# Performance work log

Measured on AMD Instinct MI355X. Metric: run time of the kernel, lower is better.

Reference implementation:

```python
import jax, jax.numpy as jnp
import numpy as np
from jax import lax

V1 = 12001   # vocab_size + 1
E = 300      # input_encoding_size
R = 1024     # rnn_size
H = 512      # att_hid_size
F = 2048     # att_feat_size
B = 64
T = 20
L = 196      # number of attention regions (14x14)


def setup_inputs() -> dict:
    key = jax.random.key(0)
    ks = jax.random.split(key, 12)
    s = 0.02
    return {
        "seq": jax.random.randint(ks[0], (B, T), 0, V1),
        "att_feats": jax.random.normal(ks[1], (B, L, F), dtype=jnp.float32),
        "embed_w": jax.random.uniform(ks[2], (V1, E), minval=-0.1, maxval=0.1),
        "ctx2att_w": jax.random.normal(ks[3], (H, F)) * s,
        "ctx2att_b": jnp.zeros((H,)),
        "h2att_w": jax.random.normal(ks[4], (H, R)) * s,
        "h2att_b": jnp.zeros((H,)),
        "alpha_w": jax.random.normal(ks[5], (1, H)) * s,
        "alpha_b": jnp.zeros((1,)),
        "i2h_w": jax.random.normal(ks[6], (5 * R, E)) * s,
        "i2h_b": jnp.zeros((5 * R,)),
        "h2h_w": jax.random.normal(ks[7], (5 * R, R)) * s,
        "h2h_b": jnp.zeros((5 * R,)),
        "a2c_w": jax.random.normal(ks[8], (2 * R, F)) * s,
        "a2c_b": jnp.zeros((2 * R,)),
        "logit_w": jax.random.uniform(ks[9], (V1, R), minval=-0.1, maxval=0.1),
        "logit_b": jnp.zeros((V1,)),
    }


def reference(seq, att_feats, embed_w, ctx2att_w, ctx2att_b, h2att_w, h2att_b,
              alpha_w, alpha_b, i2h_w, i2h_b, h2h_w, h2h_b, a2c_w, a2c_b,
              logit_w, logit_b):
    # Eval-mode dropout (identity). Faithful to core()/lstm() math.
    Bq, Tq = seq.shape
    Rr = h2h_w.shape[1]
    # p_att_feats is recomputed identically per step in the original; hoist it.
    p_att = att_feats @ ctx2att_w.T + ctx2att_b            # [B, L, H]

    def step(carry, it):
        h, c = carry
        xt = embed_w[it]                                    # [B, E]
        # additive (Bahdanau) attention over L regions
        att_h = h @ h2att_w.T + h2att_b                     # [B, H]
        dot = jnp.tanh(p_att + att_h[:, None, :])           # [B, L, H]
        e = jnp.einsum('blh,h->bl', dot, alpha_w[0]) + alpha_b[0]
        w = jax.nn.softmax(e, axis=-1)                      # [B, L]
        att_res = jnp.einsum('bl,blf->bf', w, att_feats)    # [B, F]
        # LSTM cell with maxout in_transform and context gating via a2c
        sums = xt @ i2h_w.T + i2h_b + h @ h2h_w.T + h2h_b   # [B, 5R]
        sg = jax.nn.sigmoid(sums[:, :3 * Rr])
        in_g, fg, og = sg[:, :Rr], sg[:, Rr:2 * Rr], sg[:, 2 * Rr:3 * Rr]
        itr = sums[:, 3 * Rr:] + att_res @ a2c_w.T + a2c_b  # [B, 2R]
        g = jnp.maximum(itr[:, :Rr], itr[:, Rr:])
        nc = fg * c + in_g * g
        nh = og * jnp.tanh(nc)
        logp = jax.nn.log_softmax(nh @ logit_w.T + logit_b, axis=-1)
        return (nh, nc), logp

    h0 = jnp.zeros((Bq, Rr), dtype=att_feats.dtype)
    _, logps = lax.scan(step, (h0, h0), seq.T)              # [T, B, V+1]
    return jnp.transpose(logps, (1, 0, 2))                  # [B, T, V+1]
```

## Files before the change

kernel.cpp:

```cpp
#include <hip/hip_runtime.h>
#include <math.h>

namespace {
constexpr int kV = 12001;
constexpr int kE = 300;
constexpr int kEp = 320;
constexpr int kR = 1024;
constexpr int kH = 512;
constexpr int kF = 2048;
constexpr int kB = 64;
constexpr int kT = 20;
constexpr int kL = 196;
constexpr int kNcat = 5 * kR + kH;
constexpr int kKS = 4;
constexpr int kNc2 = kH + kF;
}

typedef __attribute__((ext_vector_type(8))) short short8;
typedef __attribute__((ext_vector_type(4))) float f32x4;

#define GLB_PTR(p) ((const __attribute__((address_space(1))) void*)(p))
#define LDS_PTR(p) ((__attribute__((address_space(3))) void*)(p))

__device__ __forceinline__ unsigned short f2bf(float f) {
    unsigned u = __builtin_bit_cast(unsigned, f);
    u = (u + 0x7fffu + ((u >> 16) & 1u)) >> 16;
    return (unsigned short)u;
}
__device__ __forceinline__ float bf2f(unsigned short h) {
    unsigned u = ((unsigned)h) << 16;
    return __builtin_bit_cast(float, u);
}
__device__ __forceinline__ float fast_tanh(float x) {
    x = fminf(15.f, fmaxf(-15.f, x));
    const float e = __expf(2.f * x);
    return (e - 1.f) / (e + 1.f);
}
__device__ __forceinline__ float fast_sig(float x) {
    return 1.f / (1.f + __expf(-x));
}

__device__ __forceinline__ int xcd_swizzle(int orig, int nwg) {
    const int q = nwg >> 3, r = nwg & 7;
    const int xcd = orig & 7, lo = orig >> 3;
    return (xcd < r ? xcd * (q + 1) : r * (q + 1) + (xcd - r) * q) + lo;
}

__global__ __launch_bounds__(256)
void conv_all_kernel(const float* __restrict__ af_in,  unsigned short* __restrict__ af_out,
                     const float* __restrict__ ctx_in,
                     const float* __restrict__ lg_in,  unsigned short* __restrict__ lg_out,
                     const float* __restrict__ h2h_in, unsigned short* __restrict__ h2h_out,
                     const float* __restrict__ h2a_in, unsigned short* __restrict__ h2a_out,
                     const float* __restrict__ a2c_in, unsigned short* __restrict__ wcomb_out,
                     const float* __restrict__ emb_in, unsigned short* __restrict__ emb_out,
                     const float* __restrict__ i2h_in, unsigned short* __restrict__ i2h_out,
                     unsigned short* __restrict__ hz_out, float* __restrict__ cb_out,
                     const float* __restrict__ ctxb_in, const float* __restrict__ a2cb_in,
                     float* __restrict__ biasc_out)
{
    constexpr int c0 = kB * kL * kF / 4;
    constexpr int c1 = c0 + kH * kF / 4;
    constexpr int c2 = c1 + kV * kR / 4;
    constexpr int c3 = c2 + 5 * kR * kR / 4;
    constexpr int c4 = c3 + kH * kR / 4;
    constexpr int c5 = c4 + 2 * kR * kF / 4;
    constexpr int c6 = c5 + kV * 80;
    constexpr int c7 = c6 + 5 * kR * 80;
    constexpr int c8 = c7 + kB * kR / 4;
    constexpr int c9 = c8 + kB * kR / 4;
    constexpr int c10 = c9 + kNc2 / 4;

    for (int i = blockIdx.x * 256 + threadIdx.x; i < c10; i += gridDim.x * 256) {
        if (i < c4) {
            const float* in; unsigned short* out; int l;
            if      (i < c0) { in = af_in;  out = af_out;    l = i; }
            else if (i < c1) { in = ctx_in; out = wcomb_out; l = i - c0; }
            else if (i < c2) { in = lg_in;  out = lg_out;    l = i - c1; }
            else if (i < c3) { in = h2h_in; out = h2h_out;   l = i - c2; }
            else             { in = h2a_in; out = h2a_out;   l = i - c3; }
            const float4 v = ((const float4*)in)[l];
            ushort4 o;
            o.x = f2bf(v.x); o.y = f2bf(v.y); o.z = f2bf(v.z); o.w = f2bf(v.w);
            ((ushort4*)out)[l] = o;
        } else if (i < c5) {
            const int l = i - c4;
            const int q = l >> 9;
            const int g = l & 511;
            const int irow = (q < kR) ? (kH + 2 * q) : (kH + 2 * (q - kR) + 1);
            const float4 v = ((const float4*)a2c_in)[l];
            ushort4 o;
            o.x = f2bf(v.x); o.y = f2bf(v.y); o.z = f2bf(v.z); o.w = f2bf(v.w);
            ((ushort4*)wcomb_out)[(size_t)irow * (kF / 4) + g] = o;
        } else if (i < c7) {
            const float* in; unsigned short* out; int l;
            if (i < c6) { in = emb_in; out = emb_out; l = i - c5; }
            else        { in = i2h_in; out = i2h_out; l = i - c6; }
            const int row = l / 80, c = l - row * 80;
            ushort4 o = make_ushort4(0, 0, 0, 0);
            if (c < 75) {
                const float4 v = *(const float4*)(in + (size_t)row * kE + c * 4);
                o.x = f2bf(v.x); o.y = f2bf(v.y); o.z = f2bf(v.z); o.w = f2bf(v.w);
            }
            *(ushort4*)(out + (size_t)row * kEp + c * 4) = o;
        } else if (i < c8) {
            ((ushort4*)hz_out)[i - c7] = make_ushort4(0, 0, 0, 0);
        } else if (i < c9) {
            ((float4*)cb_out)[i - c8] = make_float4(0.f, 0.f, 0.f, 0.f);
        } else {
            const int l = i - c9;
            float4 v;
            if (l < kH / 4) {
                v = ((const float4*)ctxb_in)[l];
            } else {
                const int j0 = (l - kH / 4) * 4;
                float t[4];
                #pragma unroll
                for (int p = 0; p < 4; ++p) {
                    const int j = j0 + p;
                    const int r = j >> 1;
                    t[p] = a2cb_in[(j & 1) * kR + r];
                }
                v = make_float4(t[0], t[1], t[2], t[3]);
            }
            ((float4*)biasc_out)[l] = v;
        }
    }
}

template<bool OUT_BF16, bool GATHER>
__global__ __launch_bounds__(256)
void gemm_glds_kernel(const unsigned short* __restrict__ Ah, int lda,
                      const unsigned short* __restrict__ Wh, int ldw,
                      const float* __restrict__ bias,
                      void* __restrict__ Cp, int ldc,
                      int M, int N, int K,
                      const int* __restrict__ ridx,
                      int nbx, int nby, int nfirst)
{
    __shared__ __align__(16) unsigned short sA[128 * 32];
    __shared__ __align__(16) unsigned short sW[128 * 32];
    const int tid = threadIdx.x;
    const int swz = xcd_swizzle(blockIdx.x, nbx * nby);
    int bx, by;
    if (nfirst) { bx = swz % nbx; by = swz / nbx; }
    else        { by = swz % nby; bx = swz / nby; }
    const int m0 = by * 128;
    const int n0 = bx * 128;
    const int wave = tid >> 6, lane = tid & 63;
    const int wm = wave >> 1, wn = wave & 1;
    const int lrow = lane & 15, lkg = lane >> 4;

    const int rsub   = lane >> 2;
    const int cchunk = (lane & 3) * 8;

    f32x4 acc[4][4];
    #pragma unroll
    for (int mi = 0; mi < 4; ++mi)
        #pragma unroll
        for (int ni = 0; ni < 4; ++ni)
            acc[mi][ni] = (f32x4){0.f, 0.f, 0.f, 0.f};

    for (int k0 = 0; k0 < K; k0 += 32) {
        #pragma unroll
        for (int j = 0; j < 2; ++j) {
            const int mrow = m0 + wave * 32 + j * 16 + rsub;
            const int row = GATHER ? ridx[mrow] : mrow;
            __builtin_amdgcn_global_load_lds(
                GLB_PTR(Ah + (size_t)row * lda + k0 + cchunk),
                LDS_PTR(sA + wave * 1024 + j * 512), 16, 0, 0);
        }
        #pragma unroll
        for (int j = 0; j < 2; ++j) {
            const int n = n0 + wave * 32 + j * 16 + rsub;
            __builtin_amdgcn_global_load_lds(
                GLB_PTR(Wh + (size_t)n * ldw + k0 + cchunk),
                LDS_PTR(sW + wave * 1024 + j * 512), 16, 0, 0);
        }
        __syncthreads();

        short8 af[4], wf[4];
        #pragma unroll
        for (int mi = 0; mi < 4; ++mi)
            af[mi] = *(const short8*)(sA + (wm * 64 + mi * 16 + lrow) * 32 + lkg * 8);
        #pragma unroll
        for (int ni = 0; ni < 4; ++ni)
            wf[ni] = *(const short8*)(sW + (wn * 64 + ni * 16 + lrow) * 32 + lkg * 8);
        #pragma unroll
        for (int mi = 0; mi < 4; ++mi)
            #pragma unroll
            for (int ni = 0; ni < 4; ++ni)
                acc[mi][ni] = __builtin_amdgcn_mfma_f32_16x16x32_bf16(af[mi], wf[ni], acc[mi][ni], 0, 0, 0);
        __syncthreads();
    }

    #pragma unroll
    for (int mi = 0; mi < 4; ++mi) {
        const int mbase = m0 + wm * 64 + mi * 16 + lkg * 4;
        #pragma unroll
        for (int ni = 0; ni < 4; ++ni) {
            const int n = n0 + wn * 64 + ni * 16 + lrow;
            if (n >= N) continue;
            const float bb = bias ? bias[n] : 0.f;
            #pragma unroll
            for (int r = 0; r < 4; ++r) {
                const int m = mbase + r;
                const float v = acc[mi][ni][r] + bb;
                if (OUT_BF16) ((unsigned short*)Cp)[(size_t)m * ldc + n] = f2bf(v);
                else          ((float*)Cp)[(size_t)m * ldc + n] = v;
            }
        }
    }
}

__global__ __launch_bounds__(256)
void gemm_sums_kernel(const unsigned short* __restrict__ A, int lda,
                      const unsigned short* __restrict__ W, int ldw,
                      float* __restrict__ part, int N, int Kblk)
{
    __shared__ __align__(16) unsigned short sA[64 * 32];
    __shared__ __align__(16) unsigned short sW[64 * 32];
    const int tid = threadIdx.x;
    const int n0 = blockIdx.x * 64;
    const int ks = blockIdx.y;
    const int kbeg = ks * Kblk;
    const int wave = tid >> 6, lane = tid & 63;
    const int lrow = lane & 15, lkg = lane >> 4;
    const int rsub   = lane >> 2;
    const int cchunk = (lane & 3) * 8;

    f32x4 acc[4];
    #pragma unroll
    for (int mi = 0; mi < 4; ++mi) acc[mi] = (f32x4){0.f, 0.f, 0.f, 0.f};

    for (int k0 = kbeg; k0 < kbeg + Kblk; k0 += 32) {
        __builtin_amdgcn_global_load_lds(
            GLB_PTR(A + (size_t)(wave * 16 + rsub) * lda + k0 + cchunk),
            LDS_PTR(sA + wave * 512), 16, 0, 0);
        __builtin_amdgcn_global_load_lds(
            GLB_PTR(W + (size_t)(n0 + wave * 16 + rsub) * ldw + k0 + cchunk),
            LDS_PTR(sW + wave * 512), 16, 0, 0);
        __syncthreads();
        const short8 wf = *(const short8*)(sW + (wave * 16 + lrow) * 32 + lkg * 8);
        #pragma unroll
        for (int mi = 0; mi < 4; ++mi) {
            const short8 af = *(const short8*)(sA + (mi * 16 + lrow) * 32 + lkg * 8);
            acc[mi] = __builtin_amdgcn_mfma_f32_16x16x32_bf16(af, wf, acc[mi], 0, 0, 0);
        }
        __syncthreads();
    }

    float* po = part + (size_t)ks * 64 * N;
    const int n = n0 + wave * 16 + lrow;
    #pragma unroll
    for (int mi = 0; mi < 4; ++mi)
        #pragma unroll
        for (int rr = 0; rr < 4; ++rr)
            po[(size_t)(mi * 16 + lkg * 4 + rr) * N + n] = acc[mi][rr];
}

__global__ __launch_bounds__(512)
void att_step_kernel(const float* __restrict__ part56,
                     const float* __restrict__ h2att_b,
                     const unsigned short* __restrict__ comb_bf,
                     const float* __restrict__ alpha_w,
                     const unsigned short* __restrict__ i2h_pre_bf,
                     const float* __restrict__ h2h_b,
                     float* __restrict__ cbuf,
                     unsigned short* __restrict__ h_all_bf,
                     int t)
{
    const int fc = blockIdx.x, b = blockIdx.y;
    const int tid = threadIdx.x;
    const int wave = tid >> 6, lane = tid & 63;
    __shared__ float ahT[8][64];
    __shared__ float awT[8][64];
    __shared__ float esm[kL];
    __shared__ float wsm[kL];
    __shared__ float red2[2];

    if (tid < kH) {
        const size_t base = (size_t)b * kNcat + 5 * kR + tid;
        float v = h2att_b[tid];
        #pragma unroll
        for (int s = 0; s < kKS; ++s) v += part56[(size_t)s * 64 * kNcat + base];
        ahT[tid & 7][tid >> 3] = v;
        awT[tid & 7][tid >> 3] = alpha_w[tid];
    }
    __syncthreads();

    for (int l = wave; l < kL; l += 8) {
        const short8 pv = *(const short8*)(comb_bf + ((size_t)b * kL + l) * kNc2 + lane * 8);
        float a = 0.f;
        #pragma unroll
        for (int j = 0; j < 8; ++j)
            a += fast_tanh(bf2f(((const unsigned short*)&pv)[j]) + ahT[j][lane]) * awT[j][lane];
        #pragma unroll
        for (int off = 32; off; off >>= 1) a += __shfl_xor(a, off, 64);
        if (lane == 0) esm[l] = a;
    }
    __syncthreads();

    if (wave == 0) {
        float m = -1e30f;
        for (int l = lane; l < kL; l += 64) m = fmaxf(m, esm[l]);
        #pragma unroll
        for (int off = 32; off; off >>= 1) m = fmaxf(m, __shfl_xor(m, off, 64));
        float ssum = 0.f;
        for (int l = lane; l < kL; l += 64) ssum += __expf(esm[l] - m);
        #pragma unroll
        for (int off = 32; off; off >>= 1) ssum += __shfl_xor(ssum, off, 64);
        if (lane == 0) { red2[0] = m; red2[1] = 1.f / ssum; }
    }
    __syncthreads();
    if (tid < kL) wsm[tid] = __expf(esm[tid] - red2[0]) * red2[1];
    __syncthreads();

    const int r = fc * 256 + (tid >> 1);
    const int l0 = (tid & 1) * 98;
    float s3 = 0.f, s4 = 0.f;
    const unsigned short* base = comb_bf + ((size_t)b * kL + l0) * kNc2 + kH + 2 * r;
    #pragma unroll 7
    for (int li = 0; li < 98; ++li) {
        const ushort2 v = *(const ushort2*)(base + (size_t)li * kNc2);
        const float wl = wsm[l0 + li];
        s3 += wl * bf2f(v.x);
        s4 += wl * bf2f(v.y);
    }
    s3 += __shfl_xor(s3, 1, 64);
    s4 += __shfl_xor(s4, 1, 64);

    if ((tid & 1) == 0) {
        const unsigned short* ib = i2h_pre_bf + (size_t)(b * kT + t) * (5 * kR);
        float S0 = bf2f(ib[r])          + h2h_b[r];
        float S1 = bf2f(ib[kR + r])     + h2h_b[kR + r];
        float S2 = bf2f(ib[2 * kR + r]) + h2h_b[2 * kR + r];
        float S3 = bf2f(ib[3 * kR + r]) + h2h_b[3 * kR + r] + s3;
        float S4 = bf2f(ib[4 * kR + r]) + h2h_b[4 * kR + r] + s4;
        #pragma unroll
        for (int s = 0; s < kKS; ++s) {
            const float* p = part56 + (size_t)s * 64 * kNcat + (size_t)b * kNcat;
            S0 += p[r];
            S1 += p[kR + r];
            S2 += p[2 * kR + r];
            S3 += p[3 * kR + r];
            S4 += p[4 * kR + r];
        }

        const float ing = fast_sig(S0);
        const float fg  = fast_sig(S1);
        const float og  = fast_sig(S2);
        const float gg  = fmaxf(S3, S4);
        const int idx = b * kR + r;
        const float nc = fg * cbuf[idx] + ing * gg;
        const float nh = og * fast_tanh(nc);
        cbuf[idx] = nc;
        h_all_bf[(size_t)(b * kT + t) * kR + r] = f2bf(nh);
    }
}

__global__ __launch_bounds__(256)
void log_softmax_kernel(float* __restrict__ out)
{
    __shared__ float mred[256];
    __shared__ float sred[256];
    const int tid = threadIdx.x;
    float* row = out + (size_t)blockIdx.x * kV;

    float m = -1e30f, s = 0.f;
    for (int v = tid; v < kV; v += 256) {
        const float x = row[v];
        if (x > m) { s = s * __expf(m - x) + 1.f; m = x; }
        else        s += __expf(x - m);
    }
    mred[tid] = m; sred[tid] = s; __syncthreads();
    for (int st = 128; st > 0; st >>= 1) {
        if (tid < st) {
            const float m2 = mred[tid + st], s2 = sred[tid + st];
            const float M = fmaxf(mred[tid], m2);
            sred[tid] = sred[tid] * __expf(mred[tid] - M) + s2 * __expf(m2 - M);
            mred[tid] = M;
        }
        __syncthreads();
    }
    const float ls = mred[0] + logf(sred[0]);
    for (int v = tid; v < kV; v += 256) row[v] -= ls;
}

extern "C" void kernel_launch(void* const* d_in, const int* in_sizes, int n_in,
                              void* d_out, int out_size, void* d_ws, size_t ws_size,
                              hipStream_t stream)
{
    const int*   seq       = (const int*)  d_in[0];
    const float* att_feats = (const float*)d_in[1];
    const float* embed_w   = (const float*)d_in[2];
    const float* ctx2att_w = (const float*)d_in[3];
    const float* ctx2att_b = (const float*)d_in[4];
    const float* h2att_w   = (const float*)d_in[5];
    const float* h2att_b   = (const float*)d_in[6];
    const float* alpha_w   = (const float*)d_in[7];
    const float* i2h_w     = (const float*)d_in[9];
    const float* i2h_b     = (const float*)d_in[10];
    const float* h2h_w     = (const float*)d_in[11];
    const float* h2h_b     = (const float*)d_in[12];
    const float* a2c_w     = (const float*)d_in[13];
    const float* a2c_b     = (const float*)d_in[14];
    const float* logit_w   = (const float*)d_in[15];
    const float* logit_b   = (const float*)d_in[16];
    float* out = (float*)d_out;

    float* ws = (float*)d_ws;
    size_t off = 0;
    auto alloc = [&](size_t nf) { float* p = ws + off; off += (nf + 3) & ~(size_t)3; return p; };

    unsigned short* af_bf      = (unsigned short*)alloc((size_t)kB * kL * kF / 2);
    unsigned short* comb_bf    = (unsigned short*)alloc((size_t)kB * kL * kNc2 / 2);
    unsigned short* logit_hi   = (unsigned short*)alloc((size_t)kV * kR / 2);
    unsigned short* embed_bf   = (unsigned short*)alloc((size_t)kV * kEp / 2);
    unsigned short* i2h_bf     = (unsigned short*)alloc((size_t)5 * kR * kEp / 2);
    unsigned short* wcat_bf    = (unsigned short*)alloc((size_t)kNcat * kR / 2);
    unsigned short* wcomb_bf   = (unsigned short*)alloc((size_t)kNc2 * kF / 2);
    unsigned short* h_all_bf   = (unsigned short*)alloc((size_t)kB * kT * kR / 2);
    unsigned short* h_zero_bf  = (unsigned short*)alloc((size_t)kB * kR / 2);
    unsigned short* i2h_pre_bf = (unsigned short*)alloc((size_t)kB * kT * 5 * kR / 2);
    float* bias_comb = alloc((size_t)kNc2);
    float* part56    = alloc((size_t)kKS * kB * kNcat);
    float* cbuf      = alloc((size_t)kB * kR);

    conv_all_kernel<<<4096, 256, 0, stream>>>(
        att_feats, af_bf, ctx2att_w, logit_w, logit_hi,
        h2h_w, wcat_bf, h2att_w, wcat_bf + (size_t)5 * kR * kR,
        a2c_w, wcomb_bf, embed_w, embed_bf, i2h_w, i2h_bf,
        h_zero_bf, cbuf, ctx2att_b, a2c_b, bias_comb);

    gemm_glds_kernel<true, false><<<dim3(20 * 98), 256, 0, stream>>>(
        af_bf, kF, wcomb_bf, kF, bias_comb, comb_bf, kNc2, kB * kL, kNc2, kF, nullptr,
        20, 98, 1);

    gemm_glds_kernel<true, true><<<dim3(40 * 10), 256, 0, stream>>>(
        embed_bf, kEp, i2h_bf, kEp, i2h_b, i2h_pre_bf, 5 * kR, kB * kT, 5 * kR, kEp, seq,
        40, 10, 1);

    for (int t = 0; t < kT; ++t) {
        const unsigned short* h_prev = (t == 0) ? h_zero_bf : (h_all_bf + (size_t)(t - 1) * kR);
        const int lda_h = (t == 0) ? kR : kT * kR;

        gemm_sums_kernel<<<dim3(kNcat / 64, kKS), 256, 0, stream>>>(
            h_prev, lda_h, wcat_bf, kR, part56, kNcat, kR / kKS);

        att_step_kernel<<<dim3(4, kB), 512, 0, stream>>>(
            part56, h2att_b, comb_bf, alpha_w, i2h_pre_bf, h2h_b,
            cbuf, h_all_bf, t);
    }

    gemm_glds_kernel<false, false><<<dim3(94 * 10), 256, 0, stream>>>(
        h_all_bf, kR, logit_hi, kR, logit_b, out, kV, kB * kT, kV, kR, nullptr,
        94, 10, 0);

    log_softmax_kernel<<<dim3(kB * kT), 256, 0, stream>>>(out);
}
```

Measured before the change: 1.178 ms.

## Fuse per-step recurrent GEMM and attention/LSTM into one kernel with atomic handoff

The two kernels launched for each timestep (the split-K h-GEMM and the attention/LSTM cell) are merged into a single launch. The first 176 blocks compute the GEMM partials and bump a per-step atomic counter; the remaining blocks spin until the counter is full, then run the attention and cell update. This removes one kernel launch and its drain/fill gap per step. It relies on every producer block being resident or scheduled ahead of the spinning consumers, which risks deadlock or wasted CU time if they are not. The log-softmax kernel also moves from 256 to 512 threads per block.

```diff
diff --git a/kernel.cpp b/kernel.cpp
--- a/kernel.cpp
+++ b/kernel.cpp
@@ -14,6 +14,7 @@
 constexpr int kNcat = 5 * kR + kH;
 constexpr int kKS = 4;
 constexpr int kNc2 = kH + kF;
+constexpr int kProd = 44 * kKS;
 }
 
 typedef __attribute__((ext_vector_type(8))) short short8;
@@ -57,7 +58,7 @@
                      const float* __restrict__ i2h_in, unsigned short* __restrict__ i2h_out,
                      unsigned short* __restrict__ hz_out, float* __restrict__ cb_out,
                      const float* __restrict__ ctxb_in, const float* __restrict__ a2cb_in,
-                     float* __restrict__ biasc_out)
+                     float* __restrict__ biasc_out, unsigned* __restrict__ cnt_out)
 {
     constexpr int c0 = kB * kL * kF / 4;
     constexpr int c1 = c0 + kH * kF / 4;
@@ -70,8 +71,9 @@
     constexpr int c8 = c7 + kB * kR / 4;
     constexpr int c9 = c8 + kB * kR / 4;
     constexpr int c10 = c9 + kNc2 / 4;
-
-    for (int i = blockIdx.x * 256 + threadIdx.x; i < c10; i += gridDim.x * 256) {
+    constexpr int c11 = c10 + 8;
+
+    for (int i = blockIdx.x * 256 + threadIdx.x; i < c11; i += gridDim.x * 256) {
         if (i < c4) {
             const float* in; unsigned short* out; int l;
             if      (i < c0) { in = af_in;  out = af_out;    l = i; }
@@ -107,7 +109,7 @@
             ((ushort4*)hz_out)[i - c7] = make_ushort4(0, 0, 0, 0);
         } else if (i < c9) {
             ((float4*)cb_out)[i - c8] = make_float4(0.f, 0.f, 0.f, 0.f);
-        } else {
+        } else if (i < c10) {
             const int l = i - c9;
             float4 v;
             if (l < kH / 4) {
@@ -124,6 +126,8 @@
                 v = make_float4(t[0], t[1], t[2], t[3]);
             }
             ((float4*)biasc_out)[l] = v;
+        } else {
+            ((uint4*)cnt_out)[i - c10] = make_uint4(0u, 0u, 0u, 0u);
         }
     }
 }
@@ -213,168 +217,184 @@
     }
 }
 
-__global__ __launch_bounds__(256)
-void gemm_sums_kernel(const unsigned short* __restrict__ A, int lda,
-                      const unsigned short* __restrict__ W, int ldw,
-                      float* __restrict__ part, int N, int Kblk)
+__global__ __launch_bounds__(512)
+void step_fused_kernel(const unsigned short* __restrict__ h_prev, int lda_h,
+                       const unsigned short* __restrict__ wcat_bf,
+                       float* __restrict__ part56,
+                       const float* __restrict__ h2att_b,
+                       const unsigned short* __restrict__ comb_bf,
+                       const float* __restrict__ alpha_w,
+                       const unsigned short* __restrict__ i2h_pre_bf,
+                       const float* __restrict__ h2h_b,
+                       float* __restrict__ cbuf,
+                       unsigned short* __restrict__ h_all_bf,
+                       unsigned* __restrict__ cnt,
+                       int t)
 {
-    __shared__ __align__(16) unsigned short sA[64 * 32];
-    __shared__ __align__(16) unsigned short sW[64 * 32];
-    const int tid = threadIdx.x;
-    const int n0 = blockIdx.x * 64;
-    const int ks = blockIdx.y;
-    const int kbeg = ks * Kblk;
-    const int wave = tid >> 6, lane = tid & 63;
-    const int lrow = lane & 15, lkg = lane >> 4;
-    const int rsub   = lane >> 2;
-    const int cchunk = (lane & 3) * 8;
-
-    f32x4 acc[4];
-    #pragma unroll
-    for (int mi = 0; mi < 4; ++mi) acc[mi] = (f32x4){0.f, 0.f, 0.f, 0.f};
-
-    for (int k0 = kbeg; k0 < kbeg + Kblk; k0 += 32) {
-        __builtin_amdgcn_global_load_lds(
-            GLB_PTR(A + (size_t)(wave * 16 + rsub) * lda + k0 + cchunk),
-            LDS_PTR(sA + wave * 512), 16, 0, 0);
-        __builtin_amdgcn_global_load_lds(
-            GLB_PTR(W + (size_t)(n0 + wave * 16 + rsub) * ldw + k0 + cchunk),
-            LDS_PTR(sW + wave * 512), 16, 0, 0);
-        __syncthreads();
-        const short8 wf = *(const short8*)(sW + (wave * 16 + lrow) * 32 + lkg * 8);
-        #pragma unroll
-        for (int mi = 0; mi < 4; ++mi) {
-            const short8 af = *(const short8*)(sA + (mi * 16 + lrow) * 32 + lkg * 8);
-            acc[mi] = __builtin_amdgcn_mfma_f32_16x16x32_bf16(af, wf, acc[mi], 0, 0, 0);
-        }
-        __syncthreads();
-    }
-
-    float* po = part + (size_t)ks * 64 * N;
-    const int n = n0 + wave * 16 + lrow;
-    #pragma unroll
-    for (int mi = 0; mi < 4; ++mi)
-        #pragma unroll
-        for (int rr = 0; rr < 4; ++rr)
-            po[(size_t)(mi * 16 + lkg * 4 + rr) * N + n] = acc[mi][rr];
+    __shared__ union {
+        struct { __align__(16) unsigned short sA[2][64 * 32]; __align__(16) unsigned short sW[2][64 * 32]; } p;
+        struct { float ahT[8][64]; float awT[8][64]; float esm[kL]; float wsm[kL]; float red2[2]; } c;
+    } sm;
+
+    if (blockIdx.x < kProd) {
+        const int half = threadIdx.x >> 8;
+        const int tid = threadIdx.x & 255;
+        const int bx = blockIdx.x % 44;
+        const int ks = blockIdx.x / 44;
+        const int n0 = bx * 128 + half * 64;
+        const int kbeg = ks * (kR / kKS);
+        const int wave = tid >> 6, lane = tid & 63;
+        const int lrow = lane & 15, lkg = lane >> 4;
+        const int rsub = lane >> 2;
+        const int cchunk = (lane & 3) * 8;
+
+        f32x4 acc[4];
+        #pragma unroll
+        for (int mi = 0; mi < 4; ++mi) acc[mi] = (f32x4){0.f, 0.f, 0.f, 0.f};
+
+        unsigned short* sA = sm.p.sA[half];
+        unsigned short* sW = sm.p.sW[half];
+
+        for (int k0 = kbeg; k0 < kbeg + kR / kKS; k0 += 32) {
+            __builtin_amdgcn_global_load_lds(
+                GLB_PTR(h_prev + (size_t)(wave * 16 + rsub) * lda_h + k0 + cchunk),
+                LDS_PTR(sA + wave * 512), 16, 0, 0);
+            __builtin_amdgcn_global_load_lds(
+                GLB_PTR(wcat_bf + (size_t)(n0 + wave * 16 + rsub) * kR + k0 + cchunk),
+                LDS_PTR(sW + wave * 512), 16, 0, 0);
+            __syncthreads();
+            const short8 wf = *(const short8*)(sW + (wave * 16 + lrow) * 32 + lkg * 8);
+            #pragma unroll
+            for (int mi = 0; mi < 4; ++mi) {
+                const short8 af = *(const short8*)(sA + (mi * 16 + lrow) * 32 + lkg * 8);
+                acc[mi] = __builtin_amdgcn_mfma_f32_16x16x32_bf16(af, wf, acc[mi], 0, 0, 0);
+            }
+            __syncthreads();
+        }
+
+        float* po = part56 + (size_t)ks * 64 * kNcat;
+        const int n = n0 + wave * 16 + lrow;
+        #pragma unroll
+        for (int mi = 0; mi < 4; ++mi)
+            #pragma unroll
+            for (int rr = 0; rr < 4; ++rr)
+                po[(size_t)(mi * 16 + lkg * 4 + rr) * kNcat + n] = acc[mi][rr];
+
+        __syncthreads();
+        __threadfence();
+        if (threadIdx.x == 0)
+            __hip_atomic_fetch_add(cnt + t, 1u, __ATOMIC_RELEASE, __HIP_MEMORY_SCOPE_AGENT);
+    } else {
+        const int cblk = blockIdx.x - kProd;
+        const int fc = cblk >> 6, b = cblk & 63;
+        const int tid = threadIdx.x;
+        const int wave = tid >> 6, lane = tid & 63;
+
+        if (tid == 0) {
+            while (__hip_atomic_load(cnt + t, __ATOMIC_RELAXED, __HIP_MEMORY_SCOPE_AGENT) < (unsigned)kProd)
+                __builtin_amdgcn_s_sleep(4);
+            (void)__hip_atomic_load(cnt + t, __ATOMIC_ACQUIRE, __HIP_MEMORY_SCOPE_AGENT);
+            __threadfence();
+        }
+        __syncthreads();
+
+        if (tid < kH) {
+            const size_t base = (size_t)b * kNcat + 5 * kR + tid;
+            float v = h2att_b[tid];
+            #pragma unroll
+            for (int s = 0; s < kKS; ++s) v += part56[(size_t)s * 64 * kNcat + base];
+            sm.c.ahT[tid & 7][tid >> 3] = v;
+            sm.c.awT[tid & 7][tid >> 3] = alpha_w[tid];
+        }
+        __syncthreads();
+
+        for (int l = wave; l < kL; l += 8) {
+            const short8 pv = *(const short8*)(comb_bf + ((size_t)b * kL + l) * kNc2 + lane * 8);
+            float a = 0.f;
+            #pragma unroll
+            for (int j = 0; j < 8; ++j)
+                a += fast_tanh(bf2f(((const unsigned short*)&pv)[j]) + sm.c.ahT[j][lane]) * sm.c.awT[j][lane];
+            #pragma unroll
+            for (int off = 32; off; off >>= 1) a += __shfl_xor(a, off, 64);
+            if (lane == 0) sm.c.esm[l] = a;
+        }
+        __syncthreads();
+
+        if (wave == 0) {
+            float m = -1e30f;
+            for (int l = lane; l < kL; l += 64) m = fmaxf(m, sm.c.esm[l]);
+            #pragma unroll
+            for (int off = 32; off; off >>= 1) m = fmaxf(m, __shfl_xor(m, off, 64));
+            float ssum = 0.f;
+            for (int l = lane; l < kL; l += 64) ssum += __expf(sm.c.esm[l] - m);
+            #pragma unroll
+            for (int off = 32; off; off >>= 1) ssum += __shfl_xor(ssum, off, 64);
+            if (lane == 0) { sm.c.red2[0] = m; sm.c.red2[1] = 1.f / ssum; }
+        }
+        __syncthreads();
+        if (tid < kL) sm.c.wsm[tid] = __expf(sm.c.esm[tid] - sm.c.red2[0]) * sm.c.red2[1];
+        __syncthreads();
+
+        const int r = fc * 256 + (tid >> 1);
+        const int l0 = (tid & 1) * 98;
+        float s3 = 0.f, s4 = 0.f;
+        const unsigned short* base = comb_bf + ((size_t)b * kL + l0) * kNc2 + kH + 2 * r;
+        #pragma unroll 7
+        for (int li = 0; li < 98; ++li) {
+            const ushort2 v = *(const ushort2*)(base + (size_t)li * kNc2);
+            const float wl = sm.c.wsm[l0 + li];
+            s3 += wl * bf2f(v.x);
+            s4 += wl * bf2f(v.y);
+        }
+        s3 += __shfl_xor(s3, 1, 64);
+        s4 += __shfl_xor(s4, 1, 64);
+
+        if ((tid & 1) == 0) {
+            const unsigned short* ib = i2h_pre_bf + (size_t)(b * kT + t) * (5 * kR);
+            float S0 = bf2f(ib[r])          + h2h_b[r];
+            float S1 = bf2f(ib[kR + r])     + h2h_b[kR + r];
+            float S2 = bf2f(ib[2 * kR + r]) + h2h_b[2 * kR + r];
+            float S3 = bf2f(ib[3 * kR + r]) + h2h_b[3 * kR + r] + s3;
+            float S4 = bf2f(ib[4 * kR + r]) + h2h_b[4 * kR + r] + s4;
+            #pragma unroll
+            for (int s = 0; s < kKS; ++s) {
+                const float* p = part56 + (size_t)s * 64 * kNcat + (size_t)b * kNcat;
+                S0 += p[r];
+                S1 += p[kR + r];
+                S2 += p[2 * kR + r];
+                S3 += p[3 * kR + r];
+                S4 += p[4 * kR + r];
+            }
+
+            const float ing = fast_sig(S0);
+            const float fg  = fast_sig(S1);
+            const float og  = fast_sig(S2);
+            const float gg  = fmaxf(S3, S4);
+            const int idx = b * kR + r;
+            const float nc = fg * cbuf[idx] + ing * gg;
+            const float nh = og * fast_tanh(nc);
+            cbuf[idx] = nc;
+            h_all_bf[(size_t)(b * kT + t) * kR + r] = f2bf(nh);
+        }
+    }
 }
 
 __global__ __launch_bounds__(512)
-void att_step_kernel(const float* __restrict__ part56,
-                     const float* __restrict__ h2att_b,
-                     const unsigned short* __restrict__ comb_bf,
-                     const float* __restrict__ alpha_w,
-                     const unsigned short* __restrict__ i2h_pre_bf,
-                     const float* __restrict__ h2h_b,
-                     float* __restrict__ cbuf,
-                     unsigned short* __restrict__ h_all_bf,
-                     int t)
-{
-    const int fc = blockIdx.x, b = blockIdx.y;
-    const int tid = threadIdx.x;
-    const int wave = tid >> 6, lane = tid & 63;
-    __shared__ float ahT[8][64];
-    __shared__ float awT[8][64];
-    __shared__ float esm[kL];
-    __shared__ float wsm[kL];
-    __shared__ float red2[2];
-
-    if (tid < kH) {
-        const size_t base = (size_t)b * kNcat + 5 * kR + tid;
-        float v = h2att_b[tid];
-        #pragma unroll
-        for (int s = 0; s < kKS; ++s) v += part56[(size_t)s * 64 * kNcat + base];
-        ahT[tid & 7][tid >> 3] = v;
-        awT[tid & 7][tid >> 3] = alpha_w[tid];
-    }
-    __syncthreads();
-
-    for (int l = wave; l < kL; l += 8) {
-        const short8 pv = *(const short8*)(comb_bf + ((size_t)b * kL + l) * kNc2 + lane * 8);
-        float a = 0.f;
-        #pragma unroll
-        for (int j = 0; j < 8; ++j)
-            a += fast_tanh(bf2f(((const unsigned short*)&pv)[j]) + ahT[j][lane]) * awT[j][lane];
-        #pragma unroll
-        for (int off = 32; off; off >>= 1) a += __shfl_xor(a, off, 64);
-        if (lane == 0) esm[l] = a;
-    }
-    __syncthreads();
-
-    if (wave == 0) {
-        float m = -1e30f;
-        for (int l = lane; l < kL; l += 64) m = fmaxf(m, esm[l]);
-        #pragma unroll
-        for (int off = 32; off; off >>= 1) m = fmaxf(m, __shfl_xor(m, off, 64));
-        float ssum = 0.f;
-        for (int l = lane; l < kL; l += 64) ssum += __expf(esm[l] - m);
-        #pragma unroll
-        for (int off = 32; off; off >>= 1) ssum += __shfl_xor(ssum, off, 64);
-        if (lane == 0) { red2[0] = m; red2[1] = 1.f / ssum; }
-    }
-    __syncthreads();
-    if (tid < kL) wsm[tid] = __expf(esm[tid] - red2[0]) * red2[1];
-    __syncthreads();
-
-    const int r = fc * 256 + (tid >> 1);
-    const int l0 = (tid & 1) * 98;
-    float s3 = 0.f, s4 = 0.f;
-    const unsigned short* base = comb_bf + ((size_t)b * kL + l0) * kNc2 + kH + 2 * r;
-    #pragma unroll 7
-    for (int li = 0; li < 98; ++li) {
-        const ushort2 v = *(const ushort2*)(base + (size_t)li * kNc2);
-        const float wl = wsm[l0 + li];
-        s3 += wl * bf2f(v.x);
-        s4 += wl * bf2f(v.y);
-    }
-    s3 += __shfl_xor(s3, 1, 64);
-    s4 += __shfl_xor(s4, 1, 64);
-
-    if ((tid & 1) == 0) {
-        const unsigned short* ib = i2h_pre_bf + (size_t)(b * kT + t) * (5 * kR);
-        float S0 = bf2f(ib[r])          + h2h_b[r];
-        float S1 = bf2f(ib[kR + r])     + h2h_b[kR + r];
-        float S2 = bf2f(ib[2 * kR + r]) + h2h_b[2 * kR + r];
-        float S3 = bf2f(ib[3 * kR + r]) + h2h_b[3 * kR + r] + s3;
-        float S4 = bf2f(ib[4 * kR + r]) + h2h_b[4 * kR + r] + s4;
-        #pragma unroll
-        for (int s = 0; s < kKS; ++s) {
-            const float* p = part56 + (size_t)s * 64 * kNcat + (size_t)b * kNcat;
-            S0 += p[r];
-            S1 += p[kR + r];
-            S2 += p[2 * kR + r];
-            S3 += p[3 * kR + r];
-            S4 += p[4 * kR + r];
-        }
-
-        const float ing = fast_sig(S0);
-        const float fg  = fast_sig(S1);
-        const float og  = fast_sig(S2);
-        const float gg  = fmaxf(S3, S4);
-        const int idx = b * kR + r;
-        const float nc = fg * cbuf[idx] + ing * gg;
-        const float nh = og * fast_tanh(nc);
-        cbuf[idx] = nc;
-        h_all_bf[(size_t)(b * kT + t) * kR + r] = f2bf(nh);
-    }
-}
-
-__global__ __launch_bounds__(256)
 void log_softmax_kernel(float* __restrict__ out)
 {
-    __shared__ float mred[256];
-    __shared__ float sred[256];
+    __shared__ float mred[512];
+    __shared__ float sred[512];
     const int tid = threadIdx.x;
     float* row = out + (size_t)blockIdx.x * kV;
 
     float m = -1e30f, s = 0.f;
-    for (int v = tid; v < kV; v += 256) {
+    for (int v = tid; v < kV; v += 512) {
         const float x = row[v];
         if (x > m) { s = s * __expf(m - x) + 1.f; m = x; }
         else        s += __expf(x - m);
     }
     mred[tid] = m; sred[tid] = s; __syncthreads();
-    for (int st = 128; st > 0; st >>= 1) {
+    for (int st = 256; st > 0; st >>= 1) {
         if (tid < st) {
             const float m2 = mred[tid + st], s2 = sred[tid + st];
             const float M = fmaxf(mred[tid], m2);
@@ -384,7 +404,7 @@
         __syncthreads();
     }
     const float ls = mred[0] + logf(sred[0]);
-    for (int v = tid; v < kV; v += 256) row[v] -= ls;
+    for (int v = tid; v < kV; v += 512) row[v] -= ls;
 }
 
 extern "C" void kernel_launch(void* const* d_in, const int* in_sizes, int n_in,
@@ -426,12 +446,13 @@
     float* bias_comb = alloc((size_t)kNc2);
     float* part56    = alloc((size_t)kKS * kB * kNcat);
     float* cbuf      = alloc((size_t)kB * kR);
+    unsigned* cnt    = (unsigned*)alloc(32);
 
     conv_all_kernel<<<4096, 256, 0, stream>>>(
         att_feats, af_bf, ctx2att_w, logit_w, logit_hi,
         h2h_w, wcat_bf, h2att_w, wcat_bf + (size_t)5 * kR * kR,
         a2c_w, wcomb_bf, embed_w, embed_bf, i2h_w, i2h_bf,
-        h_zero_bf, cbuf, ctx2att_b, a2c_b, bias_comb);
+        h_zero_bf, cbuf, ctx2att_b, a2c_b, bias_comb, cnt);
 
     gemm_glds_kernel<true, false><<<dim3(20 * 98), 256, 0, stream>>>(
         af_bf, kF, wcomb_bf, kF, bias_comb, comb_bf, kNc2, kB * kL, kNc2, kF, nullptr,
@@ -444,18 +465,14 @@
     for (int t = 0; t < kT; ++t) {
         const unsigned short* h_prev = (t == 0) ? h_zero_bf : (h_all_bf + (size_t)(t - 1) * kR);
         const int lda_h = (t == 0) ? kR : kT * kR;
-
-        gemm_sums_kernel<<<dim3(kNcat / 64, kKS), 256, 0, stream>>>(
-            h_prev, lda_h, wcat_bf, kR, part56, kNcat, kR / kKS);
-
-        att_step_kernel<<<dim3(4, kB), 512, 0, stream>>>(
-            part56, h2att_b, comb_bf, alpha_w, i2h_pre_bf, h2h_b,
-            cbuf, h_all_bf, t);
+        step_fused_kernel<<<dim3(kProd + 4 * kB), 512, 0, stream>>>(
+            h_prev, lda_h, wcat_bf, part56, h2att_b, comb_bf, alpha_w,
+            i2h_pre_bf, h2h_b, cbuf, h_all_bf, cnt, t);
     }
 
     gemm_glds_kernel<false, false><<<dim3(94 * 10), 256, 0, stream>>>(
         h_all_bf, kR, logit_hi, kR, logit_b, out, kV, kB * kT, kV, kR, nullptr,
         94, 10, 0);
 
-    log_softmax_kernel<<<dim3(kB * kT), 256, 0, stream>>>(out);
-}
+    log_softmax_kernel<<<dim3(kB * kT), 512, 0, stream>>>(out);
+}
```

Result: slower. 2.224 ms (+88.7%).
